# Optimization experiments

Hardware: AMD Instinct MI355X
Metric: run time of the kernel (lower is better)

Reference implementation:

```python
import jax, jax.numpy as jnp
import numpy as np

B, T_ENC, T_DEC = 16, 256, 64
N_MEL = 80
ENC_DIM = 512
ATTN_RNN_DIM = 1024
DEC_RNN_DIM = 1024
PRENET_DIM = 256
ATTN_DIM = 128
LOC_FILTERS = 32
LOC_KERNEL = 31


def setup_inputs() -> dict:
    key = jax.random.key(0)
    ks = jax.random.split(key, 32)
    s = 0.02
    inp = {
        "memory": jax.random.normal(ks[0], (B, T_ENC, ENC_DIM), jnp.float32),
        "decoder_inputs": jax.random.normal(ks[1], (B, N_MEL, T_DEC), jnp.float32),
        "memory_lengths": jax.random.randint(ks[2], (B,), T_ENC // 2, T_ENC + 1, jnp.int32),
        # prenet
        "prenet_W1": jax.random.normal(ks[3], (PRENET_DIM, N_MEL), jnp.float32) * s,
        "prenet_b1": jnp.zeros((PRENET_DIM,), jnp.float32),
        "prenet_W2": jax.random.normal(ks[4], (PRENET_DIM, PRENET_DIM), jnp.float32) * s,
        "prenet_b2": jnp.zeros((PRENET_DIM,), jnp.float32),
        # attention LSTMCell: input = prenet_dim + enc_dim
        "attn_rnn_Wih": jax.random.normal(ks[5], (4 * ATTN_RNN_DIM, PRENET_DIM + ENC_DIM), jnp.float32) * s,
        "attn_rnn_Whh": jax.random.normal(ks[6], (4 * ATTN_RNN_DIM, ATTN_RNN_DIM), jnp.float32) * s,
        "attn_rnn_bih": jnp.zeros((4 * ATTN_RNN_DIM,), jnp.float32),
        "attn_rnn_bhh": jnp.zeros((4 * ATTN_RNN_DIM,), jnp.float32),
        # attention projections (bias-free, Tacotron2 style)
        "query_W": jax.random.normal(ks[7], (ATTN_DIM, ATTN_RNN_DIM), jnp.float32) * s,
        "mem_W": jax.random.normal(ks[8], (ATTN_DIM, ENC_DIM), jnp.float32) * s,
        "loc_conv_W": jax.random.normal(ks[9], (LOC_FILTERS, 2, LOC_KERNEL), jnp.float32) * s,
        "loc_dense_W": jax.random.normal(ks[10], (ATTN_DIM, LOC_FILTERS), jnp.float32) * s,
        "attn_v": jax.random.normal(ks[11], (1, ATTN_DIM), jnp.float32) * s,
        # decoder LSTMCell: input = attn_rnn_dim + enc_dim
        "dec_rnn_Wih": jax.random.normal(ks[12], (4 * DEC_RNN_DIM, ATTN_RNN_DIM + ENC_DIM), jnp.float32) * s,
        "dec_rnn_Whh": jax.random.normal(ks[13], (4 * DEC_RNN_DIM, DEC_RNN_DIM), jnp.float32) * s,
        "dec_rnn_bih": jnp.zeros((4 * DEC_RNN_DIM,), jnp.float32),
        "dec_rnn_bhh": jnp.zeros((4 * DEC_RNN_DIM,), jnp.float32),
        # output heads
        "proj_W": jax.random.normal(ks[14], (N_MEL, DEC_RNN_DIM + ENC_DIM), jnp.float32) * s,
        "proj_b": jnp.zeros((N_MEL,), jnp.float32),
        "gate_W": jax.random.normal(ks[15], (1, DEC_RNN_DIM + ENC_DIM), jnp.float32) * s,
        "gate_b": jnp.zeros((1,), jnp.float32),
    }
    return inp


def _lstm_cell(x, h, c, Wih, Whh, bih, bhh):
    gates = x @ Wih.T + bih + h @ Whh.T + bhh  # [B, 4H]
    i, f, g, o = jnp.split(gates, 4, axis=-1)
    c2 = jax.nn.sigmoid(f) * c + jax.nn.sigmoid(i) * jnp.tanh(g)
    h2 = jax.nn.sigmoid(o) * jnp.tanh(c2)
    return h2, c2


def _decoder_forward(memory, decoder_inputs, memory_lengths,
                     prenet_W1, prenet_b1, prenet_W2, prenet_b2,
                     attn_rnn_Wih, attn_rnn_Whh, attn_rnn_bih, attn_rnn_bhh,
                     query_W, mem_W, loc_conv_W, loc_dense_W, attn_v,
                     dec_rnn_Wih, dec_rnn_Whh, dec_rnn_bih, dec_rnn_bhh,
                     proj_W, proj_b, gate_W, gate_b):
    b, t_enc, _ = memory.shape
    t_dec = decoder_inputs.shape[2]
    # parse_decoder_inputs: [B,80,T] -> [T,B,80]; prepend go frame
    frames = jnp.transpose(decoder_inputs, (2, 0, 1))  # [T,B,80]
    go = jnp.zeros((1, b, N_MEL), frames.dtype)
    frames = jnp.concatenate([go, frames], axis=0)  # [T+1,B,80]
    # prenet (dropout disabled for determinism)
    pre = jax.nn.relu(frames @ prenet_W1.T + prenet_b1)
    pre = jax.nn.relu(pre @ prenet_W2.T + prenet_b2)  # [T+1,B,256]
    pre = pre[:-1]  # steps use frames 0..T-1

    processed_memory = memory @ mem_W.T  # [B,T_enc,128]
    pad_mask = jnp.arange(t_enc)[None, :] >= memory_lengths[:, None]  # [B,T_enc] True=pad

    pad = (LOC_KERNEL - 1) // 2

    def step(carry, x_t):
        (ah, ac, dh, dc, aw, aw_cum, ctx) = carry
        cell_in = jnp.concatenate([x_t, ctx], axis=-1)
        ah, ac = _lstm_cell(cell_in, ah, ac, attn_rnn_Wih, attn_rnn_Whh, attn_rnn_bih, attn_rnn_bhh)
        # location-sensitive attention
        awc = jnp.stack([aw, aw_cum], axis=1)  # [B,2,T_enc]
        loc = jax.lax.conv_general_dilated(
            awc, loc_conv_W, window_strides=(1,), padding=[(pad, pad)],
            dimension_numbers=("NCH", "OIH", "NCH"))  # [B,32,T_enc]
        loc = jnp.transpose(loc, (0, 2, 1)) @ loc_dense_W.T  # [B,T_enc,128]
        query = (ah @ query_W.T)[:, None, :]  # [B,1,128]
        energies = jnp.squeeze(jnp.tanh(query + processed_memory + loc) @ attn_v.T, -1)  # [B,T_enc]
        energies = jnp.where(pad_mask, -1e9, energies)
        aw = jax.nn.softmax(energies, axis=1)
        ctx = jnp.einsum("bt,btd->bd", aw, memory)
        aw_cum = aw_cum + aw
        dec_in = jnp.concatenate([ah, ctx], axis=-1)
        dh, dc = _lstm_cell(dec_in, dh, dc, dec_rnn_Wih, dec_rnn_Whh, dec_rnn_bih, dec_rnn_bhh)
        dhc = jnp.concatenate([dh, ctx], axis=-1)
        mel = dhc @ proj_W.T + proj_b  # [B,80]
        gate = jnp.squeeze(dhc @ gate_W.T + gate_b, -1)  # [B]
        return (ah, ac, dh, dc, aw, aw_cum, ctx), (mel, gate, aw)

    z = jnp.zeros
    carry0 = (z((b, ATTN_RNN_DIM)), z((b, ATTN_RNN_DIM)),
              z((b, DEC_RNN_DIM)), z((b, DEC_RNN_DIM)),
              z((b, t_enc)), z((b, t_enc)), z((b, ENC_DIM)))
    _, (mels, gates, aligns) = jax.lax.scan(step, carry0, pre)
    # parse_decoder_outputs
    mel_outputs = jnp.transpose(mels, (1, 2, 0))  # [B,80,T_dec]
    gate_outputs = jnp.transpose(gates, (1, 0))  # [B,T_dec]
    alignments = jnp.transpose(aligns, (1, 0, 2))  # [B,T_dec,T_enc]
    return mel_outputs, gate_outputs, alignments


def reference(memory, decoder_inputs, memory_lengths,
              prenet_W1, prenet_b1, prenet_W2, prenet_b2,
              attn_rnn_Wih, attn_rnn_Whh, attn_rnn_bih, attn_rnn_bhh,
              query_W, mem_W, loc_conv_W, loc_dense_W, attn_v,
              dec_rnn_Wih, dec_rnn_Whh, dec_rnn_bih, dec_rnn_bhh,
              proj_W, proj_b, gate_W, gate_b):
    return _decoder_forward(memory, decoder_inputs, memory_lengths,
                            prenet_W1, prenet_b1, prenet_W2, prenet_b2,
                            attn_rnn_Wih, attn_rnn_Whh, attn_rnn_bih, attn_rnn_bhh,
                            query_W, mem_W, loc_conv_W, loc_dense_W, attn_v,
                            dec_rnn_Wih, dec_rnn_Whh, dec_rnn_bih, dec_rnn_bhh,
                            proj_W, proj_b, gate_W, gate_b)
```

## Files before the change

kernel.cpp:

```cpp
#include <hip/hip_runtime.h>

typedef __attribute__((ext_vector_type(8))) short short8;
typedef __attribute__((ext_vector_type(4))) float f32x4;
typedef unsigned short u16;
typedef unsigned int u32;
typedef unsigned long long u64;


static constexpr size_t OFF_WFA   = 0;
static constexpr size_t OFF_WFD   = 14680064;
static constexpr size_t OFF_PREF  = 35651584;
static constexpr size_t OFF_QWB   = 36175872;
static constexpr size_t OFF_MWT   = 36438016;
static constexpr size_t OFF_BA    = 36700160;
static constexpr size_t OFF_BD    = 36716544;
static constexpr size_t OFF_PM    = 36732928;
static constexpr size_t OFF_CTXF  = 38830080;
static constexpr size_t OFF_DHF   = 40960000;
static constexpr size_t OFF_AHFD  = 45219840;
static constexpr size_t OFF_CTXFD = 47349760;
static constexpr size_t OFF_DHFD  = 48414720;
static constexpr size_t OFF_BAR   = 50544640;
static constexpr size_t OFF_END   = 50548736;

__device__ __forceinline__ float sigmf(float x) { return 1.f / (1.f + expf(-x)); }
__device__ __forceinline__ float tanh_fast(float x) {
  float e2 = __expf(2.f * x);
  return 1.f - 2.f / (e2 + 1.f);
}
__device__ __forceinline__ u16 f2bf(float f) {
  u32 u = __float_as_uint(f);
  return (u16)((u + 0x7FFFu + ((u >> 16) & 1u)) >> 16);
}
__device__ __forceinline__ float bf2f(u16 x) { return __uint_as_float(((u32)x) << 16); }

__device__ __forceinline__ short8 ld_frag_nt(const void* p) {
  const u64* q = (const u64*)p;
  u64 lo = __builtin_nontemporal_load(q);
  u64 hi = __builtin_nontemporal_load(q + 1);
  union { u64 q2[2]; short8 s; } u;
  u.q2[0] = lo; u.q2[1] = hi;
  return u.s;
}

__device__ __forceinline__ void st_u16_agent(u16* p, u16 v) {
  __hip_atomic_store(p, v, __ATOMIC_RELAXED, __HIP_MEMORY_SCOPE_AGENT);
}
__device__ __forceinline__ void st_f32_agent(float* p, float v) {
  __hip_atomic_store(p, v, __ATOMIC_RELAXED, __HIP_MEMORY_SCOPE_AGENT);
}
__device__ __forceinline__ u32 ld_u32_agent(const u32* p) {
  return __hip_atomic_load(p, __ATOMIC_RELAXED, __HIP_MEMORY_SCOPE_AGENT);
}
__device__ __forceinline__ void st_u32_agent(u32* p, u32 v) {
  __hip_atomic_store(p, v, __ATOMIC_RELAXED, __HIP_MEMORY_SCOPE_AGENT);
}

template <int SLP>
__device__ __forceinline__ void wait_p128(const u32* F, u32 target, int th) {
  if (th < 64) {
    for (;;) {
      u32 v0 = ld_u32_agent(F + th);
      u32 v1 = ld_u32_agent(F + 64 + th);
      u32 mn = v0 < v1 ? v0 : v1;
      if (__all(mn >= target)) break;
      __builtin_amdgcn_s_sleep(SLP);
    }
  }
  __syncthreads();
}
template <int SLP>
__device__ __forceinline__ void wait_s16(const u32* F, u32 target, int th) {
  if (th < 64) {
    const u32* pf = F + (th & 15) * 16;
    for (;;) {
      u32 v = ld_u32_agent(pf);
      if (__all(v >= target)) break;
      __builtin_amdgcn_s_sleep(SLP);
    }
  }
  __syncthreads();
}

__global__ void k_wfrag(const float* __restrict__ Wih, const float* __restrict__ Whh,
                        char* __restrict__ dst, int NT, int Kih) {
  int idx = blockIdx.x * 256 + threadIdx.x;
  int l = idx & 63;
  int st = idx >> 6;
  int s = st % NT, tile = st / NT;
  int r = l & 15, kg = l >> 4;
  int j = (r >> 2) * 1024 + tile * 4 + (r & 3);
  int k0 = s * 32 + kg * 8;
  const float* src = (k0 < Kih) ? (Wih + (size_t)j * Kih + k0)
                                : (Whh + (size_t)j * 1024 + (k0 - Kih));
  short8 v;
#pragma unroll
  for (int e = 0; e < 8; ++e) v[e] = (short)f2bf(src[e]);
  *(short8*)(dst + (size_t)idx * 16) = v;
}

__global__ void k_smallprep(const float* __restrict__ memW,
                            const float* __restrict__ abih, const float* __restrict__ abhh,
                            const float* __restrict__ dbih, const float* __restrict__ dbhh,
                            const float* __restrict__ qW, char* __restrict__ wsb) {
  int idx = blockIdx.x * 256 + threadIdx.x;
  if (idx < 65536) {
    int k = idx >> 7, d = idx & 127;
    ((float*)(wsb + OFF_MWT))[idx] = memW[d * 512 + k];
  } else if (idx < 69632) {
    int j = idx - 65536;
    ((float*)(wsb + OFF_BA))[j] = abih[j] + abhh[j];
  } else if (idx < 73728) {
    int j = idx - 69632;
    ((float*)(wsb + OFF_BD))[j] = dbih[j] + dbhh[j];
  } else if (idx < 204800) {
    int j = idx - 73728;
    ((u16*)(wsb + OFF_QWB))[j] = f2bf(qW[j]);
  }
}

__global__ void k_prenet(const float* __restrict__ dec_in,
                         const float* __restrict__ W1, const float* __restrict__ b1,
                         const float* __restrict__ W2, const float* __restrict__ b2,
                         char* __restrict__ wsb) {
  int s = blockIdx.x, b = blockIdx.y, th = threadIdx.x;
  __shared__ float frame[80];
  __shared__ float h1[256];
  if (th < 80) frame[th] = (s == 0) ? 0.f : dec_in[(b * 80 + th) * 64 + (s - 1)];
  __syncthreads();
  float a = b1[th];
  const float* w1r = W1 + th * 80;
  for (int m = 0; m < 80; ++m) a += w1r[m] * frame[m];
  h1[th] = fmaxf(a, 0.f);
  __syncthreads();
  float a2 = b2[th];
  const float* w2r = W2 + th * 256;
  for (int i = 0; i < 256; ++i) a2 += w2r[i] * h1[i];
  float pre = fmaxf(a2, 0.f);
  int k = th;
  ((u16*)(wsb + OFF_PREF))[(((size_t)s * 8 + (k >> 5)) * 64 + ((k >> 3) & 3) * 16 + b) * 8 + (k & 7)] = f2bf(pre);
}

__global__ void k_pm(const float* __restrict__ memory, char* __restrict__ wsb) {
  int bk = blockIdx.x, th = threadIdx.x;
  int b = bk >> 4, t0 = (bk & 15) * 16;
  __shared__ float mrow[16 * 512];
  for (int i = 0; i < 8; ++i) {
    int fi4 = i * 256 + th;
    int tl = fi4 >> 7, k4 = (fi4 & 127) << 2;
    *(float4*)&mrow[tl * 512 + k4] =
        *(const float4*)&memory[((size_t)(b * 256 + t0 + tl)) * 512 + k4];
  }
  __syncthreads();
  int d = th & 127, tl0 = th >> 7;
  float acc[8] = {};
  const float* mWT = (const float*)(wsb + OFF_MWT);
  float* pmw = (float*)(wsb + OFF_PM);
  for (int k = 0; k < 512; ++k) {
    float w = mWT[k * 128 + d];
#pragma unroll
    for (int i = 0; i < 8; ++i) acc[i] += w * mrow[(tl0 + i * 2) * 512 + k];
  }
  for (int i = 0; i < 8; ++i)
    pmw[((size_t)(b * 256 + t0 + tl0 + i * 2)) * 128 + d] = acc[i];
}

struct KParams {
  const float* memory;
  const int* mlen;
  const float* convW;
  const float* ldW;
  const float* attnv;
  const float* projW;
  const float* projb;
  const float* gateW;
  const float* gateb;
  char* wsb;
  float* out;
};

__device__ __forceinline__ void run_dec(char* wsb, int t, int tb, int th, int l, int w,
                                        int rt, int kc, float biasD_r, float& cD,
                                        float* smC) {
  const char* wfd = wsb + OFF_WFD;
  int tIdx = tb * 2 + rt;
  f32x4 acc = {0.f, 0.f, 0.f, 0.f};
#pragma unroll
  for (int i = 0; i < 20; ++i) {
    int kt = kc * 20 + i;
    short8 av = *(const short8*)(wfd + (((size_t)tIdx * 80 + kt) * 64 + l) * 16);
    const char* src;
    if (kt < 32)      src = wsb + OFF_AHFD + (((size_t)t * 32 + kt) * 64 + l) * 16;
    else if (kt < 48) src = wsb + OFF_CTXFD + (((size_t)t * 16 + (kt - 32)) * 64 + l) * 16;
    else              src = wsb + OFF_DHFD + (((size_t)(t - 1) * 32 + (kt - 48)) * 64 + l) * 16;
    short8 bv = ld_frag_nt(src);
    acc = __builtin_amdgcn_mfma_f32_16x16x32_bf16(av, bv, acc, 0, 0, 0);
  }
#pragma unroll
  for (int r4 = 0; r4 < 4; ++r4)
    smC[w * 256 + ((l >> 4) * 4 + r4) * 16 + (l & 15)] = acc[r4];
  __syncthreads();
  {
    int rt2 = th >> 8, r = (th >> 4) & 15, b2 = th & 15;
    float s = 0.f;
#pragma unroll
    for (int q = 0; q < 4; ++q) s += smC[(q * 2 + rt2) * 256 + r * 16 + b2];
    smC[4096 + th] = s + biasD_r;
  }
  __syncthreads();
  if (th < 128) {
    int b = th & 15, lu = th >> 4;
    int rt3 = lu >> 2, ul = lu & 3;
    int u = (tb * 2 + rt3) * 4 + ul;
    float gi = smC[4096 + rt3 * 256 + ul * 16 + b];
    float gf = smC[4096 + rt3 * 256 + (4 + ul) * 16 + b];
    float gc = smC[4096 + rt3 * 256 + (8 + ul) * 16 + b];
    float go = smC[4096 + rt3 * 256 + (12 + ul) * 16 + b];
    float c2 = sigmf(gf) * cD + sigmf(gi) * tanhf(gc);
    float h2 = sigmf(go) * tanhf(c2);
    cD = c2;
    st_f32_agent((float*)(wsb + OFF_DHF) + ((size_t)t * 1024 + u) * 16 + b, h2);
    st_u16_agent((u16*)(wsb + OFF_DHFD) +
                 ((((size_t)t * 32 + (u >> 5)) * 64 + ((u >> 3) & 3) * 16 + b) * 8 + (u & 7)),
                 f2bf(h2));
  }
}

__global__ void __launch_bounds__(512, 1) k_main(KParams p) {
  const int th = threadIdx.x;
  const int bk = blockIdx.x;
  char* wsb = p.wsb;
  const int l = th & 63, w = th >> 6;
  u32* Af = (u32*)(wsb + OFF_BAR);
  u32* Df = (u32*)(wsb + OFF_BAR + 1024);
  u32* Bf = (u32*)(wsb + OFF_BAR + 2048);

  __shared__ float smC[4608];
  __shared__ float s2q[128], s2v[128];
  __shared__ u16 s_convF[8192];
  __shared__ __align__(16) float s2ah[1024];
  __shared__ float s_e[256], s3wr[4];
  __shared__ float s1cw[1984];
  __shared__ float s_aw[256], s_awc[256];

  const float* pm = (const float*)(wsb + OFF_PM);
  const u16* qwb = (const u16*)(wsb + OFF_QWB);

  if (bk < 16) {
    for (int i = th; i < 1984; i += 512) s1cw[i] = p.convW[i];
    for (int i = th; i < 4096; i += 512) ((u32*)s_convF)[i] = 0u;
    if (th < 128) s2v[th] = p.attnv[th];
    if (th < 256) { s_aw[th] = 0.f; s_awc[th] = 0.f; }
  }

  float biasA_r = 0.f, biasD_r = 0.f;
  if (bk >= 16 && bk < 144) {
    int r = (th >> 4) & 15, rt2 = th >> 8, tbase = (bk - 16) * 2;
    biasA_r = ((const float*)(wsb + OFF_BA))[(r >> 2) * 1024 + (tbase + rt2) * 4 + (r & 3)];
    biasD_r = ((const float*)(wsb + OFF_BD))[(r >> 2) * 1024 + (tbase + rt2) * 4 + (r & 3)];
  }
  int lenB = 0;
  if (bk < 16) lenB = p.mlen[bk];
  float cA = 0.f, cD = 0.f;

  const int rt = w & 1, kc = w >> 1;
  short8 afA[14];
  if (bk >= 16 && bk < 144) {
    const char* wfa = wsb + OFF_WFA;
    int tIdx = (bk - 16) * 2 + rt;
#pragma unroll
    for (int i = 0; i < 14; ++i)
      afA[i] = *(const short8*)(wfa + (((size_t)tIdx * 56 + (kc * 14 + i)) * 64 + l) * 16);
  }
  short8 ldwB[8];
  if (bk < 16) {
    int kg = l >> 4, dcol = l & 15;
#pragma unroll
    for (int dt = 0; dt < 8; ++dt) {
      short8 v;
#pragma unroll
      for (int e = 0; e < 8; ++e)
        v[e] = (short)f2bf(p.ldW[(dt * 16 + dcol) * 32 + kg * 8 + e]);
      ldwB[dt] = v;
    }
  }
  __syncthreads();

  if (bk >= 16 && bk < 144) {
    const int tb = bk - 16;
    for (int t = 0; t < 64; ++t) {
      wait_s16<4>(Bf, (u32)t, th);
      {
        f32x4 acc = {0.f, 0.f, 0.f, 0.f};
#pragma unroll
        for (int i = 0; i < 14; ++i) {
          int kt = kc * 14 + i;
          const char* src;
          if (kt < 8)       src = wsb + OFF_PREF + (((size_t)t * 8 + kt) * 64 + l) * 16;
          else if (kt < 24) src = wsb + OFF_CTXFD + (((size_t)t * 16 + (kt - 8)) * 64 + l) * 16;
          else              src = wsb + OFF_AHFD + (((size_t)t * 32 + (kt - 24)) * 64 + l) * 16;
          short8 bv = ld_frag_nt(src);
          acc = __builtin_amdgcn_mfma_f32_16x16x32_bf16(afA[i], bv, acc, 0, 0, 0);
        }
#pragma unroll
        for (int r4 = 0; r4 < 4; ++r4)
          smC[w * 256 + ((l >> 4) * 4 + r4) * 16 + (l & 15)] = acc[r4];
        __syncthreads();
        {
          int rt2 = th >> 8, r = (th >> 4) & 15, b2 = th & 15;
          float s = 0.f;
#pragma unroll
          for (int q = 0; q < 4; ++q) s += smC[(q * 2 + rt2) * 256 + r * 16 + b2];
          smC[4096 + th] = s + biasA_r;
        }
        __syncthreads();
        if (th < 128) {
          int b = th & 15, lu = th >> 4;
          int rt3 = lu >> 2, ul = lu & 3;
          int u = (tb * 2 + rt3) * 4 + ul;
          float gi = smC[4096 + rt3 * 256 + ul * 16 + b];
          float gf = smC[4096 + rt3 * 256 + (4 + ul) * 16 + b];
          float gc = smC[4096 + rt3 * 256 + (8 + ul) * 16 + b];
          float go = smC[4096 + rt3 * 256 + (12 + ul) * 16 + b];
          float c2 = sigmf(gf) * cA + sigmf(gi) * tanhf(gc);
          float h2 = sigmf(go) * tanhf(c2);
          cA = c2;
          st_u16_agent((u16*)(wsb + OFF_AHFD) +
                       ((((size_t)(t + 1) * 32 + (u >> 5)) * 64 + ((u >> 3) & 3) * 16 + b) * 8 + (u & 7)),
                       f2bf(h2));
        }
      }
      __syncthreads();
      if (th == 0) st_u32_agent(Af + tb, (u32)(t + 1));
      if (t >= 1) {
        wait_p128<4>(Df, (u32)(t - 1), th);
        run_dec(wsb, t, tb, th, l, w, rt, kc, biasD_r, cD, smC);
        __syncthreads();
        if (th == 0) st_u32_agent(Df + tb, (u32)t);
      }
    }
    wait_s16<4>(Bf, 64u, th);
    wait_p128<4>(Df, 63u, th);
    run_dec(wsb, 64, tb, th, l, w, rt, kc, biasD_r, cD, smC);
    __syncthreads();
    if (th == 0) st_u32_agent(Df + tb, 64u);
  } else if (bk < 16) {
    const int b = bk;
    for (int t = 0; t < 64; ++t) {
      {
        int jmax = (lenB + 15) >> 4;
        for (int j = 0; j < jmax; ++j) {
          int idx = j * 512 + th, tt = idx >> 5, f = idx & 31;
          float a = 0.f;
          const float* w0 = s1cw + f * 62;
#pragma unroll
          for (int kk = 0; kk < 31; ++kk) {
            int pos = tt + kk - 15;
            bool ok = (pos >= 0 && pos < 256);
            float awv = ok ? s_aw[pos] : 0.f;
            float awcv = ok ? s_awc[pos] : 0.f;
            a += awv * w0[kk] + awcv * w0[31 + kk];
          }
          s_convF[(tt >> 4) * 512 + ((f >> 3) * 16 + (tt & 15)) * 8 + (f & 7)] = f2bf(a);
        }
      }
      wait_p128<4>(Af, (u32)(t + 1), th);
      if (th < 128) {
        int o = th;
        short8 v = ld_frag_nt(wsb + OFF_AHFD +
                    (((size_t)(t + 1) * 32 + (o >> 2)) * 64 + (o & 3) * 16 + b) * 16);
#pragma unroll
        for (int e = 0; e < 8; ++e) s2ah[o * 8 + e] = bf2f((u16)v[e]);
      }
      __syncthreads();
      {
        int d = th & 127, part = th >> 7;
        const u16* qr = qwb + d * 1024 + part * 256;
        const float* ah = s2ah + part * 256;
        float qa = 0.f;
        for (int kk = 0; kk < 256; kk += 8) {
          short8 v = *(const short8*)(qr + kk);
#pragma unroll
          for (int e = 0; e < 8; ++e) qa += bf2f((u16)v[e]) * ah[kk + e];
        }
        smC[part * 128 + d] = qa;
      }
      __syncthreads();
      if (th < 128) s2q[th] = smC[th] + smC[128 + th] + smC[256 + th] + smC[384 + th];
      __syncthreads();
      {
#pragma unroll
        for (int tl = 0; tl < 2; ++tl) {
          int ttile = w * 2 + tl;
          short8 afc = *(const short8*)&s_convF[ttile * 512 + l * 8];
          int dcol = l & 15;
          float e0 = 0.f, e1 = 0.f, e2 = 0.f, e3 = 0.f;
          const float* pmb = pm + ((size_t)(b * 256 + ttile * 16 + (l >> 4) * 4)) * 128 + dcol;
#pragma unroll
          for (int dt = 0; dt < 8; ++dt) {
            f32x4 S = {0.f, 0.f, 0.f, 0.f};
            S = __builtin_amdgcn_mfma_f32_16x16x32_bf16(afc, ldwB[dt], S, 0, 0, 0);
            int d = dt * 16 + dcol;
            float qd = s2q[d], vd = s2v[d];
            e0 += vd * tanh_fast(qd + pmb[dt * 16 + 0 * 128] + S[0]);
            e1 += vd * tanh_fast(qd + pmb[dt * 16 + 1 * 128] + S[1]);
            e2 += vd * tanh_fast(qd + pmb[dt * 16 + 2 * 128] + S[2]);
            e3 += vd * tanh_fast(qd + pmb[dt * 16 + 3 * 128] + S[3]);
          }
#pragma unroll
          for (int off = 8; off; off >>= 1) {
            e0 += __shfl_xor(e0, off);
            e1 += __shfl_xor(e1, off);
            e2 += __shfl_xor(e2, off);
            e3 += __shfl_xor(e3, off);
          }
          if ((l & 15) == 0) {
            int tb0 = ttile * 16 + (l >> 4) * 4;
            s_e[tb0]     = (tb0     < lenB) ? __expf(e0) : 0.f;
            s_e[tb0 + 1] = (tb0 + 1 < lenB) ? __expf(e1) : 0.f;
            s_e[tb0 + 2] = (tb0 + 2 < lenB) ? __expf(e2) : 0.f;
            s_e[tb0 + 3] = (tb0 + 3 < lenB) ? __expf(e3) : 0.f;
          }
        }
      }
      __syncthreads();
      if (th < 256) {
        float v0 = s_e[th];
#pragma unroll
        for (int off = 32; off; off >>= 1) v0 += __shfl_xor(v0, off);
        if ((th & 63) == 0) s3wr[th >> 6] = v0;
      }
      __syncthreads();
      float rden = 1.f / (s3wr[0] + s3wr[1] + s3wr[2] + s3wr[3]);
      if (th < 256) {
        float a = s_e[th] * rden;
        s_aw[th] = a;
        s_awc[th] += a;
        p.out[82944 + ((size_t)(b * 64 + t)) * 256 + th] = a;
      }
      __syncthreads();
      {
        int dq = th & 127, tg = th >> 7;
        int d0 = dq * 4;
        float a0 = 0.f, a1 = 0.f, a2 = 0.f, a3 = 0.f;
        const float* mb = p.memory + ((size_t)b * 256) * 512 + d0;
        for (int tt = tg; tt < lenB; tt += 4) {
          float4 mv = *(const float4*)(mb + (size_t)tt * 512);
          float aw = s_aw[tt];
          a0 += aw * mv.x; a1 += aw * mv.y; a2 += aw * mv.z; a3 += aw * mv.w;
        }
        smC[tg * 512 + d0]     = a0;
        smC[tg * 512 + d0 + 1] = a1;
        smC[tg * 512 + d0 + 2] = a2;
        smC[tg * 512 + d0 + 3] = a3;
      }
      __syncthreads();
      {
        int d = th;
        float ctxv = smC[d] + smC[512 + d] + smC[1024 + d] + smC[1536 + d];
        st_f32_agent((float*)(wsb + OFF_CTXF) + ((size_t)(t + 1) * 512 + d) * 16 + b, ctxv);
        st_u16_agent((u16*)(wsb + OFF_CTXFD) +
                     ((((size_t)(t + 1) * 16 + (d >> 5)) * 64 + ((d >> 3) & 3) * 16 + b) * 8 + (d & 7)),
                     f2bf(ctxv));
      }
      __syncthreads();
      if (th == 0) st_u32_agent(Bf + b * 16, (u32)(t + 1));
    }
  }

  if (bk >= 144) {
    wait_p128<96>(Df, 64u, th);
    wait_s16<96>(Bf, 64u, th);
  } else {
    wait_p128<8>(Df, 64u, th);
    wait_s16<8>(Bf, 64u, th);
  }
  {
    int t = bk & 63, pa = bk >> 6;
    const float* dh = (const float*)(wsb + OFF_DHF) + (size_t)(t + 1) * 16384;
    const float* cx = (const float*)(wsb + OFF_CTXF) + (size_t)(t + 1) * 8192;
    int lim = (pa == 3) ? 336 : 320;
    for (int idx = th; idx < lim; idx += 512) {
      if (idx < 320) {
        int mi = idx >> 4, b = idx & 15, m = pa * 20 + mi;
        const float* wr = p.projW + (size_t)m * 1536;
        float a0 = 0.f, a1 = 0.f;
#pragma unroll 8
        for (int k = 0; k < 1024; k += 2) { a0 += wr[k] * dh[k * 16 + b]; a1 += wr[k + 1] * dh[(k + 1) * 16 + b]; }
#pragma unroll 8
        for (int k = 0; k < 512; k += 2)  { a0 += wr[1024 + k] * cx[k * 16 + b]; a1 += wr[1025 + k] * cx[(k + 1) * 16 + b]; }
        p.out[((size_t)(b * 80 + m)) * 64 + t] = a0 + a1 + p.projb[m];
      } else {
        int b = idx - 320;
        float a0 = 0.f, a1 = 0.f;
#pragma unroll 8
        for (int k = 0; k < 1024; k += 2) { a0 += p.gateW[k] * dh[k * 16 + b]; a1 += p.gateW[k + 1] * dh[(k + 1) * 16 + b]; }
#pragma unroll 8
        for (int k = 0; k < 512; k += 2)  { a0 += p.gateW[1024 + k] * cx[k * 16 + b]; a1 += p.gateW[1025 + k] * cx[(k + 1) * 16 + b]; }
        p.out[81920 + b * 64 + t] = a0 + a1 + p.gateb[0];
      }
    }
  }
}

extern "C" void kernel_launch(void* const* d_in, const int* in_sizes, int n_in,
                              void* d_out, int out_size, void* d_ws, size_t ws_size,
                              hipStream_t stream) {
  (void)in_sizes; (void)n_in; (void)out_size; (void)ws_size;
  const float* memory = (const float*)d_in[0];
  const float* dec_in = (const float*)d_in[1];
  const int*   mlen   = (const int*)d_in[2];
  const float* pW1    = (const float*)d_in[3];
  const float* pb1    = (const float*)d_in[4];
  const float* pW2    = (const float*)d_in[5];
  const float* pb2    = (const float*)d_in[6];
  const float* aWih   = (const float*)d_in[7];
  const float* aWhh   = (const float*)d_in[8];
  const float* abih   = (const float*)d_in[9];
  const float* abhh   = (const float*)d_in[10];
  const float* qW     = (const float*)d_in[11];
  const float* memW   = (const float*)d_in[12];
  const float* convW  = (const float*)d_in[13];
  const float* ldW    = (const float*)d_in[14];
  const float* attnv  = (const float*)d_in[15];
  const float* dWih   = (const float*)d_in[16];
  const float* dWhh   = (const float*)d_in[17];
  const float* dbih   = (const float*)d_in[18];
  const float* dbhh   = (const float*)d_in[19];
  const float* projW  = (const float*)d_in[20];
  const float* projb  = (const float*)d_in[21];
  const float* gateW  = (const float*)d_in[22];
  const float* gateb  = (const float*)d_in[23];
  char* wsb = (char*)d_ws;
  float* out = (float*)d_out;

  hipMemsetAsync(wsb + OFF_AHFD, 0, 32768, stream);
  hipMemsetAsync(wsb + OFF_CTXFD, 0, 16384, stream);
  hipMemsetAsync(wsb + OFF_DHFD, 0, 32768, stream);
  hipMemsetAsync(wsb + OFF_BAR, 0, 4096, stream);

  hipLaunchKernelGGL(k_wfrag, dim3(3584), dim3(256), 0, stream, aWih, aWhh, wsb + OFF_WFA, 56, 768);
  hipLaunchKernelGGL(k_wfrag, dim3(5120), dim3(256), 0, stream, dWih, dWhh, wsb + OFF_WFD, 80, 1536);
  hipLaunchKernelGGL(k_smallprep, dim3(800), dim3(256), 0, stream, memW, abih, abhh, dbih, dbhh, qW, wsb);
  hipLaunchKernelGGL(k_prenet, dim3(64, 16), dim3(256), 0, stream, dec_in, pW1, pb1, pW2, pb2, wsb);
  hipLaunchKernelGGL(k_pm, dim3(256), dim3(256), 0, stream, memory, wsb);

  KParams p{memory, mlen, convW, ldW, attnv, projW, projb, gateW, gateb, wsb, out};
  void* args[] = { &p };
  hipLaunchCooperativeKernel((void*)k_main, dim3(256), dim3(512), args, 0, stream);
}
```

Measured before the change: 2.855 ms.

## Split attention LSTM GEMM to precompute prenet/hidden part before context arrives

The attention-RNN gate GEMM is split into an early part (prenet and previous attention hidden state) and a late part (context vector). The early part for step t+1 runs right after the decoder step, once all attention blocks have published h, so only the 4 context k-tiles remain after waiting on the attention-block flag. This shortens the critical path between the context producer and the LSTM gate update. The cost is an extra all-block wait on the Af flags each step, plus more register pressure from holding the accumulator across iterations.

Result: no change. 2.826 ms (-1.0%).

```diff
diff --git a/kernel.cpp b/kernel.cpp
--- a/kernel.cpp
+++ b/kernel.cpp
@@ -179,6 +179,21 @@
   float* out;
 };
 
+__device__ __forceinline__ f32x4 attn_early(char* wsb, int t, int kc, int l,
+                                            const short8* afE) {
+  f32x4 acc = {0.f, 0.f, 0.f, 0.f};
+#pragma unroll
+  for (int i = 0; i < 10; ++i) {
+    int pe = kc * 10 + i;
+    const char* src = (pe < 8)
+        ? wsb + OFF_PREF + (((size_t)t * 8 + pe) * 64 + l) * 16
+        : wsb + OFF_AHFD + (((size_t)t * 32 + (pe - 8)) * 64 + l) * 16;
+    short8 bv = ld_frag_nt(src);
+    acc = __builtin_amdgcn_mfma_f32_16x16x32_bf16(afE[i], bv, acc, 0, 0, 0);
+  }
+  return acc;
+}
+
 __device__ __forceinline__ void run_dec(char* wsb, int t, int tb, int th, int l, int w,
                                         int rt, int kc, float biasD_r, float& cD,
                                         float* smC) {
@@ -264,13 +279,21 @@
   float cA = 0.f, cD = 0.f;
 
   const int rt = w & 1, kc = w >> 1;
-  short8 afA[14];
+  short8 afE[10], afL[4];
   if (bk >= 16 && bk < 144) {
     const char* wfa = wsb + OFF_WFA;
     int tIdx = (bk - 16) * 2 + rt;
 #pragma unroll
-    for (int i = 0; i < 14; ++i)
-      afA[i] = *(const short8*)(wfa + (((size_t)tIdx * 56 + (kc * 14 + i)) * 64 + l) * 16);
+    for (int i = 0; i < 10; ++i) {
+      int pe = kc * 10 + i;
+      int kt = (pe < 8) ? pe : (24 + (pe - 8));
+      afE[i] = *(const short8*)(wfa + (((size_t)tIdx * 56 + kt) * 64 + l) * 16);
+    }
+#pragma unroll
+    for (int i = 0; i < 4; ++i) {
+      int kt = 8 + kc * 4 + i;
+      afL[i] = *(const short8*)(wfa + (((size_t)tIdx * 56 + kt) * 64 + l) * 16);
+    }
   }
   short8 ldwB[8];
   if (bk < 16) {
@@ -288,47 +311,41 @@
 
   if (bk >= 16 && bk < 144) {
     const int tb = bk - 16;
+    f32x4 acc = attn_early(wsb, 0, kc, l, afE);
     for (int t = 0; t < 64; ++t) {
       wait_s16<4>(Bf, (u32)t, th);
+#pragma unroll
+      for (int i = 0; i < 4; ++i) {
+        int ct = kc * 4 + i;
+        short8 bv = ld_frag_nt(wsb + OFF_CTXFD + (((size_t)t * 16 + ct) * 64 + l) * 16);
+        acc = __builtin_amdgcn_mfma_f32_16x16x32_bf16(afL[i], bv, acc, 0, 0, 0);
+      }
+#pragma unroll
+      for (int r4 = 0; r4 < 4; ++r4)
+        smC[w * 256 + ((l >> 4) * 4 + r4) * 16 + (l & 15)] = acc[r4];
+      __syncthreads();
       {
-        f32x4 acc = {0.f, 0.f, 0.f, 0.f};
-#pragma unroll
-        for (int i = 0; i < 14; ++i) {
-          int kt = kc * 14 + i;
-          const char* src;
-          if (kt < 8)       src = wsb + OFF_PREF + (((size_t)t * 8 + kt) * 64 + l) * 16;
-          else if (kt < 24) src = wsb + OFF_CTXFD + (((size_t)t * 16 + (kt - 8)) * 64 + l) * 16;
-          else              src = wsb + OFF_AHFD + (((size_t)t * 32 + (kt - 24)) * 64 + l) * 16;
-          short8 bv = ld_frag_nt(src);
-          acc = __builtin_amdgcn_mfma_f32_16x16x32_bf16(afA[i], bv, acc, 0, 0, 0);
-        }
-#pragma unroll
-        for (int r4 = 0; r4 < 4; ++r4)
-          smC[w * 256 + ((l >> 4) * 4 + r4) * 16 + (l & 15)] = acc[r4];
-        __syncthreads();
-        {
-          int rt2 = th >> 8, r = (th >> 4) & 15, b2 = th & 15;
-          float s = 0.f;
-#pragma unroll
-          for (int q = 0; q < 4; ++q) s += smC[(q * 2 + rt2) * 256 + r * 16 + b2];
-          smC[4096 + th] = s + biasA_r;
-        }
-        __syncthreads();
-        if (th < 128) {
-          int b = th & 15, lu = th >> 4;
-          int rt3 = lu >> 2, ul = lu & 3;
-          int u = (tb * 2 + rt3) * 4 + ul;
-          float gi = smC[4096 + rt3 * 256 + ul * 16 + b];
-          float gf = smC[4096 + rt3 * 256 + (4 + ul) * 16 + b];
-          float gc = smC[4096 + rt3 * 256 + (8 + ul) * 16 + b];
-          float go = smC[4096 + rt3 * 256 + (12 + ul) * 16 + b];
-          float c2 = sigmf(gf) * cA + sigmf(gi) * tanhf(gc);
-          float h2 = sigmf(go) * tanhf(c2);
-          cA = c2;
-          st_u16_agent((u16*)(wsb + OFF_AHFD) +
-                       ((((size_t)(t + 1) * 32 + (u >> 5)) * 64 + ((u >> 3) & 3) * 16 + b) * 8 + (u & 7)),
-                       f2bf(h2));
-        }
+        int rt2 = th >> 8, r = (th >> 4) & 15, b2 = th & 15;
+        float s = 0.f;
+#pragma unroll
+        for (int q = 0; q < 4; ++q) s += smC[(q * 2 + rt2) * 256 + r * 16 + b2];
+        smC[4096 + th] = s + biasA_r;
+      }
+      __syncthreads();
+      if (th < 128) {
+        int b = th & 15, lu = th >> 4;
+        int rt3 = lu >> 2, ul = lu & 3;
+        int u = (tb * 2 + rt3) * 4 + ul;
+        float gi = smC[4096 + rt3 * 256 + ul * 16 + b];
+        float gf = smC[4096 + rt3 * 256 + (4 + ul) * 16 + b];
+        float gc = smC[4096 + rt3 * 256 + (8 + ul) * 16 + b];
+        float go = smC[4096 + rt3 * 256 + (12 + ul) * 16 + b];
+        float c2 = sigmf(gf) * cA + sigmf(gi) * tanhf(gc);
+        float h2 = sigmf(go) * tanhf(c2);
+        cA = c2;
+        st_u16_agent((u16*)(wsb + OFF_AHFD) +
+                     ((((size_t)(t + 1) * 32 + (u >> 5)) * 64 + ((u >> 3) & 3) * 16 + b) * 8 + (u & 7)),
+                     f2bf(h2));
       }
       __syncthreads();
       if (th == 0) st_u32_agent(Af + tb, (u32)(t + 1));
@@ -337,6 +354,10 @@
         run_dec(wsb, t, tb, th, l, w, rt, kc, biasD_r, cD, smC);
         __syncthreads();
         if (th == 0) st_u32_agent(Df + tb, (u32)t);
+      }
+      if (t < 63) {
+        wait_p128<4>(Af, (u32)(t + 1), th);
+        acc = attn_early(wsb, t + 1, kc, l, afE);
       }
     }
     wait_s16<4>(Bf, 64u, th);
```
